# Kernel tuning notes

Hardware: AMD Instinct MI355X
Metric: run time of the kernel (lower is better)

The kernel has to match this reference:

```python
import jax, jax.numpy as jnp
import numpy as np

N_TYPES = 4
N_RELS = 8
N, E, IN_DIM, OUT_DIM = 100000, 1600000, 64, 64
SQRT_DK = float(np.sqrt(OUT_DIM))  # num_heads = 1 -> d_k = out_dim


def setup_inputs() -> dict:
    key = jax.random.key(0)
    ks = jax.random.split(key, 12)
    s = 0.05  # keep activations well-scaled (xavier-ish)
    h = jax.random.normal(ks[0], (N, IN_DIM), jnp.float32)
    node_type = jax.random.randint(ks[1], (N,), 0, N_TYPES, jnp.int32)
    src = jax.random.randint(ks[2], (E,), 0, N, jnp.int32)
    dst = jax.random.randint(ks[3], (E,), 0, N, jnp.int32)
    etype = jax.random.randint(ks[4], (E,), 0, N_RELS, jnp.int32)
    k_lin = jax.random.normal(ks[5], (N_TYPES, IN_DIM, OUT_DIM), jnp.float32) * s
    q_lin = jax.random.normal(ks[6], (N_TYPES, IN_DIM, OUT_DIM), jnp.float32) * s
    v_lin = jax.random.normal(ks[7], (N_TYPES, IN_DIM, OUT_DIM), jnp.float32) * s
    a_lin = jax.random.normal(ks[8], (N_TYPES, OUT_DIM, OUT_DIM), jnp.float32) * s
    rel_att = jax.random.normal(ks[9], (N_RELS, OUT_DIM, OUT_DIM), jnp.float32) * s
    rel_msg = jax.random.normal(ks[10], (N_RELS, OUT_DIM, OUT_DIM), jnp.float32) * s
    rel_pri = jnp.ones((N_RELS,), jnp.float32)
    skip = jnp.ones((N_TYPES,), jnp.float32)
    return dict(h=h, node_type=node_type, src=src, dst=dst, etype=etype,
                k_lin=k_lin, q_lin=q_lin, v_lin=v_lin, a_lin=a_lin,
                rel_att=rel_att, rel_msg=rel_msg, rel_pri=rel_pri, skip=skip)


def _typed_matmul(x, W, node_type):
    # rgnn_relational_matmul_no_scatter_gather_list: per-node-type GEMM.
    # Small fixed loop over node types (4), masked accumulate.
    out = jnp.zeros((x.shape[0], W.shape[-1]), x.dtype)
    for t in range(W.shape[0]):
        out = out + jnp.where((node_type == t)[:, None], x @ W[t], 0.0)
    return out


def reference(h, node_type, src, dst, etype, k_lin, q_lin, v_lin, a_lin,
              rel_att, rel_msg, rel_pri, skip):
    # per-node-type K/Q/V projections (num_heads==1, d_k==out_dim)
    k = _typed_matmul(h, k_lin, node_type)  # [N, d_k]
    q = _typed_matmul(h, q_lin, node_type)  # [N, d_k]
    v = _typed_matmul(h, v_lin, node_type)  # [N, d_k]

    # q @ relation_att, computed per relation for ALL nodes then gathered per edge
    # (avoids materializing [E, d_k, d_k] relation weights per edge)
    qW = jnp.einsum('nd,rde->rne', q, rel_att)  # [R, N, d_k]
    t_edge = qW[etype, dst]                      # [E, d_k]  (dst-side product)
    # attention score: <q_dst @ W_att_r, k_src>
    score = jnp.sum(t_edge * k[src], axis=-1)    # [E]

    # edge softmax over incoming edges of each dst, scaled by pri/sqrt(d_k)
    logits = score * (rel_pri / SQRT_DK)[etype]
    m = jax.ops.segment_max(logits, dst, num_segments=N)
    ex = jnp.exp(logits - m[dst])
    den = jax.ops.segment_sum(ex, dst, num_segments=N)
    alpha = ex / jnp.where(den[dst] == 0, 1.0, den[dst])  # [E]

    # message: v_src @ W_msg_r, per relation then gathered per edge
    vW = jnp.einsum('nd,rde->rne', v, rel_msg)   # [R, N, d_k]
    msg = vW[etype, src]                          # [E, d_k]

    # softmax-weighted aggregation to dst nodes
    agg = jax.ops.segment_sum(alpha[:, None] * msg, dst, num_segments=N)  # [N, d_k]

    # output per-node-type GEMM with sigmoid(skip)-scaled a_linears
    W_out = jax.nn.sigmoid(skip)[:, None, None] * a_lin
    return _typed_matmul(agg, W_out, node_type)  # [N, out_dim]
```

## Files before the change

kernel.cpp:

```cpp
#include <hip/hip_runtime.h>
#include <math.h>

#define DIM 64
#define NT 4
#define NR 8

typedef __attribute__((ext_vector_type(8))) short bf16x8;
typedef __attribute__((ext_vector_type(8))) unsigned short u16x8;
typedef __attribute__((ext_vector_type(4))) float f32x4;

__device__ __forceinline__ unsigned short f2bf(float f) {
    unsigned u = __float_as_uint(f);
    return (unsigned short)((u + 0x7FFF + ((u >> 16) & 1)) >> 16);
}
__device__ __forceinline__ float bf2f(unsigned short u) {
    return __uint_as_float((unsigned)u << 16);
}
__device__ __forceinline__ bf16x8 ldb16(const unsigned short* p) {
    return *((const bf16x8*)p);
}

__global__ void type_count(const int* __restrict__ ntype, int* __restrict__ tm, int N) {
    int i = blockIdx.x * blockDim.x + threadIdx.x;
    int t = (i < N) ? ntype[i] : -1;
    int lane = threadIdx.x & 63;
    #pragma unroll
    for (int tt = 0; tt < NT; tt++) {
        unsigned long long m = __ballot(t == tt);
        int c = __popcll(m);
        if (c && lane == (__ffsll((long long)m) - 1)) atomicAdd(&tm[tt], c);
    }
}

__global__ void type_scan(int* __restrict__ tm) {
    if (threadIdx.x == 0 && blockIdx.x == 0) {
        int b = 0;
        for (int t = 0; t < NT; t++) { tm[4 + t] = b; b += ((tm[t] + 63) >> 6) << 6; }
        tm[12] = b;
    }
}

__global__ void type_scatter(const int* __restrict__ ntype, int* __restrict__ tm,
                             int* __restrict__ order, int N) {
    int i = blockIdx.x * blockDim.x + threadIdx.x;
    int t = (i < N) ? ntype[i] : -1;
    int lane = threadIdx.x & 63;
    #pragma unroll
    for (int tt = 0; tt < NT; tt++) {
        unsigned long long m = __ballot(t == tt);
        int c = __popcll(m);
        if (!c) continue;
        int ldr = __ffsll((long long)m) - 1;
        int base = 0;
        if (lane == ldr) base = atomicAdd(&tm[8 + tt], c);
        base = __shfl(base, ldr, 64);
        if (t == tt) {
            int rank = __popcll(m & ((1ull << lane) - 1ull));
            order[tm[4 + tt] + base + rank] = i;
        }
    }
}

__global__ void prep_all(const float* __restrict__ A, const float* __restrict__ Mw,
                         const float* __restrict__ kl, const float* __restrict__ ql,
                         const float* __restrict__ vl,
                         unsigned short* __restrict__ At, unsigned short* __restrict__ Mt,
                         unsigned short* __restrict__ Wkt, unsigned short* __restrict__ Wqt,
                         unsigned short* __restrict__ Wvt) {
    int i = blockIdx.x * blockDim.x + threadIdx.x;
    if (i >= 28 * DIM * DIM) return;
    int mat = i >> 12;
    int idx = i & 4095;
    int n = idx >> 6;
    int k = idx & 63;
    int so = k * DIM + n;
    if (mat < 8)       At [((size_t)mat << 12) + idx]        = f2bf(A [((size_t)mat << 12) + so]);
    else if (mat < 16) Mt [((size_t)(mat - 8) << 12) + idx]  = f2bf(Mw[((size_t)(mat - 8) << 12) + so]);
    else if (mat < 20) Wkt[((size_t)(mat - 16) << 12) + idx] = f2bf(kl[((size_t)(mat - 16) << 12) + so]);
    else if (mat < 24) Wqt[((size_t)(mat - 20) << 12) + idx] = f2bf(ql[((size_t)(mat - 20) << 12) + so]);
    else               Wvt[((size_t)(mat - 24) << 12) + idx] = f2bf(vl[((size_t)(mat - 24) << 12) + so]);
}

__global__ void __launch_bounds__(256)
proj_mfma(const float* __restrict__ h, const int* __restrict__ ntype,
          const int* __restrict__ order, const int* __restrict__ tm,
          const unsigned short* __restrict__ Wkt, const unsigned short* __restrict__ Wqt,
          const unsigned short* __restrict__ Wvt,
          unsigned short* __restrict__ kvbf, unsigned short* __restrict__ qbf, int N) {
    __shared__ __align__(16) unsigned short xs[64][72];
    int t  = threadIdx.x;
    int n0 = blockIdx.x * 64;
    if (n0 >= tm[12]) return;
    int first = order[n0];
    if (first < 0) return;
    int ty = ntype[first];

    #pragma unroll
    for (int i = 0; i < 4; i++) {
        int idx = t + 256 * i;
        int row = idx >> 4, c4 = idx & 15;
        int gn = order[n0 + row];
        float4 xv = make_float4(0.f, 0.f, 0.f, 0.f);
        if (gn >= 0) xv = ((const float4*)(h + (size_t)gn * DIM))[c4];
        ushort4 b = make_ushort4(f2bf(xv.x), f2bf(xv.y), f2bf(xv.z), f2bf(xv.w));
        *((ushort4*)&xs[row][c4 * 4]) = b;
    }
    __syncthreads();

    int wave = t >> 6, lane = t & 63;
    int m = lane & 15, quad = lane >> 4;
    bf16x8 xa0 = *((const bf16x8*)&xs[wave * 16 + m][quad * 8]);
    bf16x8 xa1 = *((const bf16x8*)&xs[wave * 16 + m][32 + quad * 8]);

    int g[4];
    #pragma unroll
    for (int reg = 0; reg < 4; reg++) g[reg] = order[n0 + wave * 16 + quad * 4 + reg];

    const unsigned short* Wt[3] = { Wkt + (size_t)ty * 4096,
                                    Wqt + (size_t)ty * 4096,
                                    Wvt + (size_t)ty * 4096 };
    for (int mm = 0; mm < 3; mm++) {
        const unsigned short* W = Wt[mm];
        f32x4 c0 = {0.f,0.f,0.f,0.f}, c1 = c0, c2 = c0, c3 = c0;
        c0 = __builtin_amdgcn_mfma_f32_16x16x32_bf16(xa0, ldb16(W + (( 0 + m) << 6)      + quad * 8), c0, 0, 0, 0);
        c1 = __builtin_amdgcn_mfma_f32_16x16x32_bf16(xa0, ldb16(W + ((16 + m) << 6)      + quad * 8), c1, 0, 0, 0);
        c2 = __builtin_amdgcn_mfma_f32_16x16x32_bf16(xa0, ldb16(W + ((32 + m) << 6)      + quad * 8), c2, 0, 0, 0);
        c3 = __builtin_amdgcn_mfma_f32_16x16x32_bf16(xa0, ldb16(W + ((48 + m) << 6)      + quad * 8), c3, 0, 0, 0);
        c0 = __builtin_amdgcn_mfma_f32_16x16x32_bf16(xa1, ldb16(W + (( 0 + m) << 6) + 32 + quad * 8), c0, 0, 0, 0);
        c1 = __builtin_amdgcn_mfma_f32_16x16x32_bf16(xa1, ldb16(W + ((16 + m) << 6) + 32 + quad * 8), c1, 0, 0, 0);
        c2 = __builtin_amdgcn_mfma_f32_16x16x32_bf16(xa1, ldb16(W + ((32 + m) << 6) + 32 + quad * 8), c2, 0, 0, 0);
        c3 = __builtin_amdgcn_mfma_f32_16x16x32_bf16(xa1, ldb16(W + ((48 + m) << 6) + 32 + quad * 8), c3, 0, 0, 0);

        #pragma unroll
        for (int reg = 0; reg < 4; reg++) {
            if (g[reg] < 0) continue;
            unsigned short* row;
            if (mm == 1)       row = qbf  + ((size_t)g[reg] << 6) + m;
            else if (mm == 0)  row = kvbf + ((size_t)g[reg] << 7) + m;
            else               row = kvbf + ((size_t)g[reg] << 7) + 64 + m;
            row[ 0] = f2bf(c0[reg]);
            row[16] = f2bf(c1[reg]);
            row[32] = f2bf(c2[reg]);
            row[48] = f2bf(c3[reg]);
        }
    }
}

__global__ void hist8(const int* __restrict__ dst, const int* __restrict__ et,
                      int* __restrict__ cnt, int E) {
    int e = blockIdx.x * blockDim.x + threadIdx.x;
    if (e < E) atomicAdd(&cnt[dst[e] * NR + et[e]], 1);
}

__global__ void scan1(const int* __restrict__ cnt, int* __restrict__ off,
                      int* __restrict__ bsum, int M) {
    __shared__ int buf[1024];
    int tid = threadIdx.x;
    int i = blockIdx.x * 1024 + tid;
    int x = (i < M) ? cnt[i] : 0;
    buf[tid] = x;
    __syncthreads();
    for (int s = 1; s < 1024; s <<= 1) {
        int t = (tid >= s) ? buf[tid - s] : 0;
        __syncthreads();
        buf[tid] += t;
        __syncthreads();
    }
    if (i < M) off[i] = buf[tid] - x;
    if (tid == 1023) bsum[blockIdx.x] = buf[1023];
}

__global__ void scan2(int* __restrict__ bsum, int nb) {
    __shared__ int buf[1024];
    __shared__ int carry;
    int tid = threadIdx.x;
    if (tid == 0) carry = 0;
    __syncthreads();
    for (int base = 0; base < nb; base += 1024) {
        int i = base + tid;
        int x = (i < nb) ? bsum[i] : 0;
        buf[tid] = x;
        __syncthreads();
        for (int s = 1; s < 1024; s <<= 1) {
            int t = (tid >= s) ? buf[tid - s] : 0;
            __syncthreads();
            buf[tid] += t;
            __syncthreads();
        }
        if (i < nb) bsum[i] = carry + buf[tid] - x;
        __syncthreads();
        if (tid == 1023) carry += buf[1023];
        __syncthreads();
    }
}

__global__ void scan3(int* __restrict__ off, const int* __restrict__ bsum, int M, int E) {
    int i = blockIdx.x * 1024 + threadIdx.x;
    if (i < M) off[i] += bsum[blockIdx.x];
    if (i == 0) off[M] = E;
}

__global__ void scatter8(const int* __restrict__ src, const int* __restrict__ dst,
                         const int* __restrict__ et, const int* __restrict__ off,
                         int* __restrict__ cnt2, int* __restrict__ se, int E) {
    int e = blockIdx.x * blockDim.x + threadIdx.x;
    if (e >= E) return;
    int key = dst[e] * NR + et[e];
    int p = off[key] + atomicAdd(&cnt2[key], 1);
    se[p] = src[e];
}

__global__ void __launch_bounds__(256)
fused_edge(const unsigned short* __restrict__ qbf,
           const unsigned short* __restrict__ kvbf,
           const unsigned short* __restrict__ At,
           const unsigned short* __restrict__ Mt,
           const int* __restrict__ se, const int* __restrict__ off8,
           const float* __restrict__ rel_pri,
           float* __restrict__ agg, int N) {
    __shared__ __align__(16) unsigned short qwb[4][16][72];
    __shared__ __align__(16) unsigned short pl[4][16][72];
    const int t    = threadIdx.x;
    const int wave = t >> 6;
    const int lane = t & 63;
    const int m    = lane & 15;
    const int quad = lane >> 4;
    const int sg   = lane >> 2;
    const int ll   = lane & 3;
    const int n0   = blockIdx.x * 64 + wave * 16;
    if (n0 >= N) return;

    bf16x8 qa0 = {0,0,0,0,0,0,0,0}, qa1 = {0,0,0,0,0,0,0,0};
    {
        const int gn = n0 + m;
        if (gn < N) {
            const unsigned short* qp = qbf + ((size_t)gn << 6) + quad * 8;
            qa0 = *((const bf16x8*)qp);
            qa1 = *((const bf16x8*)(qp + 32));
        }
    }

    const int ob = n0 * NR;
    const int ov0 = off8[ob + lane];
    const int ov1 = off8[ob + 64 + lane];
    const int ov2 = off8[ob + 128];
    const bool act = (n0 + sg) < N;

    f32x4 u0 = {0.f,0.f,0.f,0.f}, u1 = u0, u2 = u0, u3 = u0;
    float ddsum = 0.f;

    for (int r = 0; r < NR; r++) {
        const unsigned short* Ar = At + ((size_t)r << 12);
        f32x4 c0 = {0.f,0.f,0.f,0.f}, c1 = c0, c2 = c0, c3 = c0;
        c0 = __builtin_amdgcn_mfma_f32_16x16x32_bf16(qa0, ldb16(Ar + (( 0 + m) << 6)      + quad * 8), c0, 0, 0, 0);
        c1 = __builtin_amdgcn_mfma_f32_16x16x32_bf16(qa0, ldb16(Ar + ((16 + m) << 6)      + quad * 8), c1, 0, 0, 0);
        c2 = __builtin_amdgcn_mfma_f32_16x16x32_bf16(qa0, ldb16(Ar + ((32 + m) << 6)      + quad * 8), c2, 0, 0, 0);
        c3 = __builtin_amdgcn_mfma_f32_16x16x32_bf16(qa0, ldb16(Ar + ((48 + m) << 6)      + quad * 8), c3, 0, 0, 0);
        c0 = __builtin_amdgcn_mfma_f32_16x16x32_bf16(qa1, ldb16(Ar + (( 0 + m) << 6) + 32 + quad * 8), c0, 0, 0, 0);
        c1 = __builtin_amdgcn_mfma_f32_16x16x32_bf16(qa1, ldb16(Ar + ((16 + m) << 6) + 32 + quad * 8), c1, 0, 0, 0);
        c2 = __builtin_amdgcn_mfma_f32_16x16x32_bf16(qa1, ldb16(Ar + ((32 + m) << 6) + 32 + quad * 8), c2, 0, 0, 0);
        c3 = __builtin_amdgcn_mfma_f32_16x16x32_bf16(qa1, ldb16(Ar + ((48 + m) << 6) + 32 + quad * 8), c3, 0, 0, 0);

        #pragma unroll
        for (int reg = 0; reg < 4; reg++) {
            unsigned short* qr = &qwb[wave][quad * 4 + reg][m];
            qr[ 0] = f2bf(c0[reg]); qr[16] = f2bf(c1[reg]);
            qr[32] = f2bf(c2[reg]); qr[48] = f2bf(c3[reg]);
        }
        asm volatile("s_waitcnt lgkmcnt(0)" ::: "memory");

        const int g  = sg * NR + r;
        const int g1 = g + 1;
        const int x0a = __shfl(ov0, g, 64);
        const int x0b = __shfl(ov1, g - 64, 64);
        int i0 = (g < 64) ? x0a : x0b;
        const int x1a = __shfl(ov0, g1, 64);
        const int x1b = __shfl(ov1, g1 - 64, 64);
        int i1 = (g1 < 64) ? x1a : ((g1 < 128) ? x1b : ov2);
        if (!act) i1 = i0;

        const float pri = rel_pri[r] * 0.125f;
        float pe[16], po[16];
        #pragma unroll
        for (int x = 0; x < 16; x++) { pe[x] = 0.f; po[x] = 0.f; }
        float dde = 0.f, ddo = 0.f;

        if (i0 < i1) {
            const u16x8 tq0 = *((const u16x8*)&qwb[wave][sg][ll * 16]);
            const u16x8 tq1 = *((const u16x8*)&qwb[wave][sg][ll * 16 + 8]);
            float tq[16];
            #pragma unroll
            for (int x = 0; x < 8; x++) { tq[x] = bf2f(tq0[x]); tq[8 + x] = bf2f(tq1[x]); }

            for (int i = i0; i < i1; i += 2) {
                const int sA = se[i];
                const bool hB = (i + 1 < i1);
                const int sB = se[hB ? i + 1 : i];
                const unsigned short* pA = kvbf + ((size_t)sA << 7) + ll * 16;
                const unsigned short* pB = kvbf + ((size_t)sB << 7) + ll * 16;
                const u16x8 kA0 = *((const u16x8*)pA);
                const u16x8 kA1 = *((const u16x8*)(pA + 8));
                const u16x8 vA0 = *((const u16x8*)(pA + 64));
                const u16x8 vA1 = *((const u16x8*)(pA + 72));
                const u16x8 kB0 = *((const u16x8*)pB);
                const u16x8 kB1 = *((const u16x8*)(pB + 8));
                const u16x8 vB0 = *((const u16x8*)(pB + 64));
                const u16x8 vB1 = *((const u16x8*)(pB + 72));
                float sa = 0.f, sb = 0.f;
                #pragma unroll
                for (int x = 0; x < 8; x++) {
                    sa = fmaf(bf2f(kA0[x]), tq[x],     sa);
                    sa = fmaf(bf2f(kA1[x]), tq[8 + x], sa);
                    sb = fmaf(bf2f(kB0[x]), tq[x],     sb);
                    sb = fmaf(bf2f(kB1[x]), tq[8 + x], sb);
                }
                sa += __shfl_xor(sa, 1, 4);
                sa += __shfl_xor(sa, 2, 4);
                sb += __shfl_xor(sb, 1, 4);
                sb += __shfl_xor(sb, 2, 4);
                const float eA = __expf(sa * pri);
                const float eB = hB ? __expf(sb * pri) : 0.f;
                dde += eA; ddo += eB;
                #pragma unroll
                for (int x = 0; x < 8; x++) {
                    pe[x]     = fmaf(eA, bf2f(vA0[x]), pe[x]);
                    pe[8 + x] = fmaf(eA, bf2f(vA1[x]), pe[8 + x]);
                    po[x]     = fmaf(eB, bf2f(vB0[x]), po[x]);
                    po[8 + x] = fmaf(eB, bf2f(vB1[x]), po[8 + x]);
                }
            }
        }
        u16x8 w0, w1;
        #pragma unroll
        for (int x = 0; x < 8; x++) {
            w0[x] = f2bf(pe[x] + po[x]);
            w1[x] = f2bf(pe[8 + x] + po[8 + x]);
        }
        *((u16x8*)&pl[wave][sg][ll * 16])     = w0;
        *((u16x8*)&pl[wave][sg][ll * 16 + 8]) = w1;
        ddsum += dde + ddo;
        asm volatile("s_waitcnt lgkmcnt(0)" ::: "memory");

        const unsigned short* Mr = Mt + ((size_t)r << 12);
        const bf16x8 pa0 = *((const bf16x8*)&pl[wave][m][quad * 8]);
        const bf16x8 pa1 = *((const bf16x8*)&pl[wave][m][32 + quad * 8]);
        u0 = __builtin_amdgcn_mfma_f32_16x16x32_bf16(pa0, ldb16(Mr + (( 0 + m) << 6)      + quad * 8), u0, 0, 0, 0);
        u1 = __builtin_amdgcn_mfma_f32_16x16x32_bf16(pa0, ldb16(Mr + ((16 + m) << 6)      + quad * 8), u1, 0, 0, 0);
        u2 = __builtin_amdgcn_mfma_f32_16x16x32_bf16(pa0, ldb16(Mr + ((32 + m) << 6)      + quad * 8), u2, 0, 0, 0);
        u3 = __builtin_amdgcn_mfma_f32_16x16x32_bf16(pa0, ldb16(Mr + ((48 + m) << 6)      + quad * 8), u3, 0, 0, 0);
        u0 = __builtin_amdgcn_mfma_f32_16x16x32_bf16(pa1, ldb16(Mr + (( 0 + m) << 6) + 32 + quad * 8), u0, 0, 0, 0);
        u1 = __builtin_amdgcn_mfma_f32_16x16x32_bf16(pa1, ldb16(Mr + ((16 + m) << 6) + 32 + quad * 8), u1, 0, 0, 0);
        u2 = __builtin_amdgcn_mfma_f32_16x16x32_bf16(pa1, ldb16(Mr + ((32 + m) << 6) + 32 + quad * 8), u2, 0, 0, 0);
        u3 = __builtin_amdgcn_mfma_f32_16x16x32_bf16(pa1, ldb16(Mr + ((48 + m) << 6) + 32 + quad * 8), u3, 0, 0, 0);
        asm volatile("s_waitcnt lgkmcnt(0)" ::: "memory");
    }

    #pragma unroll
    for (int reg = 0; reg < 4; reg++) {
        const int n = n0 + quad * 4 + reg;
        if (n >= N) continue;
        const float dv  = __shfl(ddsum, (quad * 4 + reg) << 2, 64);
        const float inv = (dv == 0.f) ? 0.f : 1.f / dv;
        float* rowp = agg + ((size_t)n << 6) + m;
        rowp[ 0] = u0[reg] * inv;
        rowp[16] = u1[reg] * inv;
        rowp[32] = u2[reg] * inv;
        rowp[48] = u3[reg] * inv;
    }
}

__global__ void out_typed(const float* __restrict__ agg, const int* __restrict__ ntype,
                          const int* __restrict__ order, const int* __restrict__ tm,
                          const float* __restrict__ Wa, const float* __restrict__ skip,
                          float* __restrict__ out, int N) {
    __shared__ float xs[64][68];
    __shared__ float wsm[64][64];
    int t  = threadIdx.x;
    int n0 = blockIdx.x * 64;
    if (n0 >= tm[12]) return;
    int first = order[n0];
    if (first < 0) return;
    int ty = ntype[first];
    float sg = 1.f / (1.f + expf(-skip[ty]));

    const float4* wg = (const float4*)(Wa + (size_t)ty * DIM * DIM);
    float4* wl = (float4*)&wsm[0][0];
    #pragma unroll
    for (int i = 0; i < 4; i++) {
        float4 w = wg[t + 256 * i];
        w.x *= sg; w.y *= sg; w.z *= sg; w.w *= sg;
        wl[t + 256 * i] = w;
    }
    #pragma unroll
    for (int i = 0; i < 4; i++) {
        int idx = t + 256 * i;
        int row = idx >> 4, c4 = idx & 15;
        int gn = order[n0 + row];
        float4 xv = make_float4(0.f, 0.f, 0.f, 0.f);
        if (gn >= 0) xv = ((const float4*)(agg + (size_t)gn * DIM))[c4];
        ((float4*)&xs[row][0])[c4] = xv;
    }
    __syncthreads();

    int og  = t & 15;
    int ng4 = (t >> 4) * 4;
    float4 a0 = make_float4(0.f,0.f,0.f,0.f), a1 = a0, a2 = a0, a3 = a0;
    #pragma unroll 8
    for (int d = 0; d < DIM; d++) {
        float4 wv = ((const float4*)&wsm[d][0])[og];
        float x0 = xs[ng4 + 0][d];
        float x1 = xs[ng4 + 1][d];
        float x2 = xs[ng4 + 2][d];
        float x3 = xs[ng4 + 3][d];
        a0.x = fmaf(x0, wv.x, a0.x); a0.y = fmaf(x0, wv.y, a0.y);
        a0.z = fmaf(x0, wv.z, a0.z); a0.w = fmaf(x0, wv.w, a0.w);
        a1.x = fmaf(x1, wv.x, a1.x); a1.y = fmaf(x1, wv.y, a1.y);
        a1.z = fmaf(x1, wv.z, a1.z); a1.w = fmaf(x1, wv.w, a1.w);
        a2.x = fmaf(x2, wv.x, a2.x); a2.y = fmaf(x2, wv.y, a2.y);
        a2.z = fmaf(x2, wv.z, a2.z); a2.w = fmaf(x2, wv.w, a2.w);
        a3.x = fmaf(x3, wv.x, a3.x); a3.y = fmaf(x3, wv.y, a3.y);
        a3.z = fmaf(x3, wv.z, a3.z); a3.w = fmaf(x3, wv.w, a3.w);
    }
    int g0 = order[n0 + ng4 + 0];
    int g1 = order[n0 + ng4 + 1];
    int g2 = order[n0 + ng4 + 2];
    int g3 = order[n0 + ng4 + 3];
    if (g0 >= 0) ((float4*)(out + (size_t)g0 * DIM))[og] = a0;
    if (g1 >= 0) ((float4*)(out + (size_t)g1 * DIM))[og] = a1;
    if (g2 >= 0) ((float4*)(out + (size_t)g2 * DIM))[og] = a2;
    if (g3 >= 0) ((float4*)(out + (size_t)g3 * DIM))[og] = a3;
}

extern "C" void kernel_launch(void* const* d_in, const int* in_sizes, int n_in,
                              void* d_out, int out_size, void* d_ws, size_t ws_size,
                              hipStream_t stream) {
    const float* h       = (const float*)d_in[0];
    const int*   ntype   = (const int*)  d_in[1];
    const int*   src     = (const int*)  d_in[2];
    const int*   dst     = (const int*)  d_in[3];
    const int*   et      = (const int*)  d_in[4];
    const float* k_lin   = (const float*)d_in[5];
    const float* q_lin   = (const float*)d_in[6];
    const float* v_lin   = (const float*)d_in[7];
    const float* a_lin   = (const float*)d_in[8];
    const float* rel_att = (const float*)d_in[9];
    const float* rel_msg = (const float*)d_in[10];
    const float* rel_pri = (const float*)d_in[11];
    const float* skip    = (const float*)d_in[12];

    int N = in_sizes[1];
    int E = in_sizes[2];
    int M = N * NR;
    int ocap = N + NT * 64;

    float* ws = (float*)d_ws;
    size_t o = 0;
    unsigned short* kvbf = (unsigned short*)(ws + o); o += (size_t)N * DIM;
    unsigned short* qbf  = (unsigned short*)(ws + o); o += (size_t)N * DIM / 2;
    float* agg  = ws + o; o += (size_t)N * DIM;
    int* off8   = (int*)(ws + o); o += (size_t)M + 1024;
    int* cnt8   = (int*)(ws + o); o += (size_t)M;
    int* cnt28  = (int*)(ws + o); o += (size_t)M;
    int* se     = (int*)(ws + o); o += (size_t)E;
    int* bsum   = (int*)(ws + o); o += 1024;
    int* order  = (int*)(ws + o); o += (size_t)ocap;
    int* tm     = (int*)(ws + o); o += 16;
    unsigned short* At  = (unsigned short*)(ws + o); o += (size_t)NR * DIM * DIM / 2;
    unsigned short* Mt  = (unsigned short*)(ws + o); o += (size_t)NR * DIM * DIM / 2;
    unsigned short* Wkt = (unsigned short*)(ws + o); o += (size_t)NT * DIM * DIM / 2;
    unsigned short* Wqt = (unsigned short*)(ws + o); o += (size_t)NT * DIM * DIM / 2;
    unsigned short* Wvt = (unsigned short*)(ws + o); o += (size_t)NT * DIM * DIM / 2;

    float* out = (float*)d_out;

    hipMemsetAsync(order, 0xFF, (size_t)ocap * 4, stream);
    hipMemsetAsync(tm, 0, 16 * 4, stream);
    hipMemsetAsync(cnt8, 0, (size_t)2 * M * 4, stream);

    type_count<<<(N + 255) / 256, 256, 0, stream>>>(ntype, tm, N);
    type_scan<<<1, 64, 0, stream>>>(tm);
    type_scatter<<<(N + 255) / 256, 256, 0, stream>>>(ntype, tm, order, N);

    prep_all<<<(28 * DIM * DIM + 255) / 256, 256, 0, stream>>>(
        rel_att, rel_msg, k_lin, q_lin, v_lin, At, Mt, Wkt, Wqt, Wvt);

    int gridT = (N + NT * 64 + 63) / 64;
    proj_mfma<<<gridT, 256, 0, stream>>>(h, ntype, order, tm, Wkt, Wqt, Wvt,
                                         kvbf, qbf, N);

    hist8<<<(E + 255) / 256, 256, 0, stream>>>(dst, et, cnt8, E);
    int nb = (M + 1023) / 1024;
    scan1<<<nb, 1024, 0, stream>>>(cnt8, off8, bsum, M);
    scan2<<<1, 1024, 0, stream>>>(bsum, nb);
    scan3<<<nb, 1024, 0, stream>>>(off8, bsum, M, E);
    scatter8<<<(E + 255) / 256, 256, 0, stream>>>(src, dst, et, off8, cnt28, se, E);

    int nb64 = (N + 63) / 64;
    fused_edge<<<nb64, 256, 0, stream>>>(qbf, kvbf, At, Mt, se, off8,
                                         rel_pri, agg, N);

    out_typed<<<gridT, 256, 0, stream>>>(agg, ntype, order, tm, a_lin, skip, out, N);
}
```

Baseline: 654.7 us.

## Fold memsets into kernels, reuse histogram ranks in scatter, shuffle-based scans

After: 611.2 us. -6.6%, faster.

```diff
diff --git a/kernel.cpp b/kernel.cpp
--- a/kernel.cpp
+++ b/kernel.cpp
@@ -20,8 +20,33 @@
     return *((const bf16x8*)p);
 }
 
-__global__ void type_count(const int* __restrict__ ntype, int* __restrict__ tm, int N) {
+__global__ void prep_all(const float* __restrict__ A, const float* __restrict__ Mw,
+                         const float* __restrict__ kl, const float* __restrict__ ql,
+                         const float* __restrict__ vl,
+                         unsigned short* __restrict__ At, unsigned short* __restrict__ Mt,
+                         unsigned short* __restrict__ Wkt, unsigned short* __restrict__ Wqt,
+                         unsigned short* __restrict__ Wvt,
+                         int* __restrict__ cnt8, int* __restrict__ tm, int M) {
     int i = blockIdx.x * blockDim.x + threadIdx.x;
+    if (i < M) cnt8[i] = 0;
+    if (i < 16) tm[i] = 0;
+    if (i >= 28 * DIM * DIM) return;
+    int mat = i >> 12;
+    int idx = i & 4095;
+    int n = idx >> 6;
+    int k = idx & 63;
+    int so = k * DIM + n;
+    if (mat < 8)       At [((size_t)mat << 12) + idx]        = f2bf(A [((size_t)mat << 12) + so]);
+    else if (mat < 16) Mt [((size_t)(mat - 8) << 12) + idx]  = f2bf(Mw[((size_t)(mat - 8) << 12) + so]);
+    else if (mat < 20) Wkt[((size_t)(mat - 16) << 12) + idx] = f2bf(kl[((size_t)(mat - 16) << 12) + so]);
+    else if (mat < 24) Wqt[((size_t)(mat - 20) << 12) + idx] = f2bf(ql[((size_t)(mat - 20) << 12) + so]);
+    else               Wvt[((size_t)(mat - 24) << 12) + idx] = f2bf(vl[((size_t)(mat - 24) << 12) + so]);
+}
+
+__global__ void type_count(const int* __restrict__ ntype, int* __restrict__ tm,
+                           int* __restrict__ order, int N, int ocap) {
+    int i = blockIdx.x * blockDim.x + threadIdx.x;
+    if (i < ocap) order[i] = -1;
     int t = (i < N) ? ntype[i] : -1;
     int lane = threadIdx.x & 63;
     #pragma unroll
@@ -59,26 +84,6 @@
             order[tm[4 + tt] + base + rank] = i;
         }
     }
-}
-
-__global__ void prep_all(const float* __restrict__ A, const float* __restrict__ Mw,
-                         const float* __restrict__ kl, const float* __restrict__ ql,
-                         const float* __restrict__ vl,
-                         unsigned short* __restrict__ At, unsigned short* __restrict__ Mt,
-                         unsigned short* __restrict__ Wkt, unsigned short* __restrict__ Wqt,
-                         unsigned short* __restrict__ Wvt) {
-    int i = blockIdx.x * blockDim.x + threadIdx.x;
-    if (i >= 28 * DIM * DIM) return;
-    int mat = i >> 12;
-    int idx = i & 4095;
-    int n = idx >> 6;
-    int k = idx & 63;
-    int so = k * DIM + n;
-    if (mat < 8)       At [((size_t)mat << 12) + idx]        = f2bf(A [((size_t)mat << 12) + so]);
-    else if (mat < 16) Mt [((size_t)(mat - 8) << 12) + idx]  = f2bf(Mw[((size_t)(mat - 8) << 12) + so]);
-    else if (mat < 20) Wkt[((size_t)(mat - 16) << 12) + idx] = f2bf(kl[((size_t)(mat - 16) << 12) + so]);
-    else if (mat < 24) Wqt[((size_t)(mat - 20) << 12) + idx] = f2bf(ql[((size_t)(mat - 20) << 12) + so]);
-    else               Wvt[((size_t)(mat - 24) << 12) + idx] = f2bf(vl[((size_t)(mat - 24) << 12) + so]);
 }
 
 __global__ void __launch_bounds__(256)
@@ -147,49 +152,73 @@
 }
 
 __global__ void hist8(const int* __restrict__ dst, const int* __restrict__ et,
-                      int* __restrict__ cnt, int E) {
+                      int* __restrict__ cnt, int* __restrict__ rank, int E) {
     int e = blockIdx.x * blockDim.x + threadIdx.x;
-    if (e < E) atomicAdd(&cnt[dst[e] * NR + et[e]], 1);
+    if (e < E) rank[e] = atomicAdd(&cnt[dst[e] * NR + et[e]], 1);
 }
 
 __global__ void scan1(const int* __restrict__ cnt, int* __restrict__ off,
                       int* __restrict__ bsum, int M) {
-    __shared__ int buf[1024];
+    __shared__ int wsum[16];
     int tid = threadIdx.x;
+    int lane = tid & 63, wid = tid >> 6;
     int i = blockIdx.x * 1024 + tid;
-    int x = (i < M) ? cnt[i] : 0;
-    buf[tid] = x;
+    int x0 = (i < M) ? cnt[i] : 0;
+    int x = x0;
+    #pragma unroll
+    for (int s = 1; s < 64; s <<= 1) {
+        int y = __shfl_up(x, s, 64);
+        if (lane >= s) x += y;
+    }
+    if (lane == 63) wsum[wid] = x;
     __syncthreads();
-    for (int s = 1; s < 1024; s <<= 1) {
-        int t = (tid >= s) ? buf[tid - s] : 0;
-        __syncthreads();
-        buf[tid] += t;
-        __syncthreads();
-    }
-    if (i < M) off[i] = buf[tid] - x;
-    if (tid == 1023) bsum[blockIdx.x] = buf[1023];
+    if (tid < 16) {
+        int w = wsum[tid];
+        #pragma unroll
+        for (int s = 1; s < 16; s <<= 1) {
+            int y = __shfl_up(w, s, 16);
+            if (tid >= s) w += y;
+        }
+        wsum[tid] = w;
+    }
+    __syncthreads();
+    int add = (wid > 0) ? wsum[wid - 1] : 0;
+    if (i < M) off[i] = add + x - x0;
+    if (tid == 1023) bsum[blockIdx.x] = wsum[15];
 }
 
 __global__ void scan2(int* __restrict__ bsum, int nb) {
-    __shared__ int buf[1024];
+    __shared__ int wsum[16];
     __shared__ int carry;
     int tid = threadIdx.x;
+    int lane = tid & 63, wid = tid >> 6;
     if (tid == 0) carry = 0;
     __syncthreads();
     for (int base = 0; base < nb; base += 1024) {
         int i = base + tid;
-        int x = (i < nb) ? bsum[i] : 0;
-        buf[tid] = x;
+        int x0 = (i < nb) ? bsum[i] : 0;
+        int x = x0;
+        #pragma unroll
+        for (int s = 1; s < 64; s <<= 1) {
+            int y = __shfl_up(x, s, 64);
+            if (lane >= s) x += y;
+        }
+        if (lane == 63) wsum[wid] = x;
         __syncthreads();
-        for (int s = 1; s < 1024; s <<= 1) {
-            int t = (tid >= s) ? buf[tid - s] : 0;
-            __syncthreads();
-            buf[tid] += t;
-            __syncthreads();
-        }
-        if (i < nb) bsum[i] = carry + buf[tid] - x;
+        if (tid < 16) {
+            int w = wsum[tid];
+            #pragma unroll
+            for (int s = 1; s < 16; s <<= 1) {
+                int y = __shfl_up(w, s, 16);
+                if (tid >= s) w += y;
+            }
+            wsum[tid] = w;
+        }
         __syncthreads();
-        if (tid == 1023) carry += buf[1023];
+        int add = carry + ((wid > 0) ? wsum[wid - 1] : 0);
+        if (i < nb) bsum[i] = add + x - x0;
+        __syncthreads();
+        if (tid == 0) carry += wsum[15];
         __syncthreads();
     }
 }
@@ -202,12 +231,11 @@
 
 __global__ void scatter8(const int* __restrict__ src, const int* __restrict__ dst,
                          const int* __restrict__ et, const int* __restrict__ off,
-                         int* __restrict__ cnt2, int* __restrict__ se, int E) {
+                         const int* __restrict__ rank, int* __restrict__ se, int E) {
     int e = blockIdx.x * blockDim.x + threadIdx.x;
     if (e >= E) return;
     int key = dst[e] * NR + et[e];
-    int p = off[key] + atomicAdd(&cnt2[key], 1);
-    se[p] = src[e];
+    se[off[key] + rank[e]] = src[e];
 }
 
 __global__ void __launch_bounds__(256)
@@ -243,7 +271,8 @@
     const int ob = n0 * NR;
     const int ov0 = off8[ob + lane];
     const int ov1 = off8[ob + 64 + lane];
-    const int ov2 = off8[ob + 128];
+    const int eeidx = ((n0 + 16 < N) ? (n0 + 16) : N) * NR;
+    const int ov2 = off8[eeidx];
     const bool act = (n0 + sg) < N;
 
     f32x4 u0 = {0.f,0.f,0.f,0.f}, u1 = u0, u2 = u0, u3 = u0;
@@ -460,7 +489,7 @@
     float* agg  = ws + o; o += (size_t)N * DIM;
     int* off8   = (int*)(ws + o); o += (size_t)M + 1024;
     int* cnt8   = (int*)(ws + o); o += (size_t)M;
-    int* cnt28  = (int*)(ws + o); o += (size_t)M;
+    int* rank   = (int*)(ws + o); o += (size_t)E;
     int* se     = (int*)(ws + o); o += (size_t)E;
     int* bsum   = (int*)(ws + o); o += 1024;
     int* order  = (int*)(ws + o); o += (size_t)ocap;
@@ -473,27 +502,24 @@
 
     float* out = (float*)d_out;
 
-    hipMemsetAsync(order, 0xFF, (size_t)ocap * 4, stream);
-    hipMemsetAsync(tm, 0, 16 * 4, stream);
-    hipMemsetAsync(cnt8, 0, (size_t)2 * M * 4, stream);
-
-    type_count<<<(N + 255) / 256, 256, 0, stream>>>(ntype, tm, N);
+    int gprep = (M > 28 * DIM * DIM ? M : 28 * DIM * DIM);
+    prep_all<<<(gprep + 255) / 256, 256, 0, stream>>>(
+        rel_att, rel_msg, k_lin, q_lin, v_lin, At, Mt, Wkt, Wqt, Wvt, cnt8, tm, M);
+
+    type_count<<<(ocap + 255) / 256, 256, 0, stream>>>(ntype, tm, order, N, ocap);
     type_scan<<<1, 64, 0, stream>>>(tm);
     type_scatter<<<(N + 255) / 256, 256, 0, stream>>>(ntype, tm, order, N);
-
-    prep_all<<<(28 * DIM * DIM + 255) / 256, 256, 0, stream>>>(
-        rel_att, rel_msg, k_lin, q_lin, v_lin, At, Mt, Wkt, Wqt, Wvt);
 
     int gridT = (N + NT * 64 + 63) / 64;
     proj_mfma<<<gridT, 256, 0, stream>>>(h, ntype, order, tm, Wkt, Wqt, Wvt,
                                          kvbf, qbf, N);
 
-    hist8<<<(E + 255) / 256, 256, 0, stream>>>(dst, et, cnt8, E);
+    hist8<<<(E + 255) / 256, 256, 0, stream>>>(dst, et, cnt8, rank, E);
     int nb = (M + 1023) / 1024;
     scan1<<<nb, 1024, 0, stream>>>(cnt8, off8, bsum, M);
     scan2<<<1, 1024, 0, stream>>>(bsum, nb);
     scan3<<<nb, 1024, 0, stream>>>(off8, bsum, M, E);
-    scatter8<<<(E + 255) / 256, 256, 0, stream>>>(src, dst, et, off8, cnt28, se, E);
+    scatter8<<<(E + 255) / 256, 256, 0, stream>>>(src, dst, et, off8, rank, se, E);
 
     int nb64 = (N + 63) / 64;
     fused_edge<<<nb64, 256, 0, stream>>>(qbf, kvbf, At, Mt, se, off8,
```
